# Kernel optimization log

Hardware: AMD Instinct MI355X
Metric: run time of the kernel (lower is better)

## Reference

```python
import jax, jax.numpy as jnp
import numpy as np

B, N, M, K = 4, 8192, 2048, 8
F1, F2 = 256, 256


def _knn_idx(p1t, p2t, k):
    # p1t [B,N,3], p2t [B,M,3] -> idx [B,N,k] of k nearest points in p2t for each p1t point
    d = (jnp.sum(p1t ** 2, -1)[:, :, None]
         + jnp.sum(p2t ** 2, -1)[:, None, :]
         - 2.0 * jnp.einsum('bnc,bmc->bnm', p1t, p2t))
    _, idx = jax.lax.top_k(-d, k)
    return idx


def _gather(feat, idx):
    # feat [B,C,M], idx [B,N,K] -> [B,C,N,K]  (grouping_operation)
    return jax.vmap(lambda f, i: f[:, i])(feat, idx)


def setup_inputs() -> dict:
    key = jax.random.key(0)
    ks = jax.random.split(key, 16)
    rn = lambda k, s: jax.random.normal(k, s, dtype=jnp.float32)
    ru = lambda k, s: jax.random.uniform(k, s, dtype=jnp.float32)
    return {
        'pos1': rn(ks[0], (B, 3, N)),
        'pos2': rn(ks[1], (B, 3, M)),
        'feature1': rn(ks[2], (B, F1, N)),
        'feature2': rn(ks[3], (B, F2, M)),
        'w1_0': rn(ks[4], (128, F2 + 3)) * 0.05, 's1_0': ru(ks[5], (128,)), 'b1_0': rn(ks[6], (128,)) * 0.05,
        'w1_1': rn(ks[7], (128, 128)) * 0.05, 's1_1': ru(ks[8], (128,)), 'b1_1': rn(ks[9], (128,)) * 0.05,
        'w1_2': rn(ks[10], (256, 128)) * 0.05, 's1_2': ru(ks[11], (256,)), 'b1_2': rn(ks[12], (256,)) * 0.05,
        'w2_0': rn(ks[13], (256, 256 + F1)) * 0.05, 's2_0': ru(ks[14], (256,)), 'b2_0': rn(ks[15], (256,)) * 0.05,
    }


def reference(pos1, pos2, feature1, feature2,
              w1_0, s1_0, b1_0, w1_1, s1_1, b1_1, w1_2, s1_2, b1_2,
              w2_0, s2_0, b2_0):
    # KNN grouping (knn=True branch): neighbors of each pos1 point among pos2 points
    idx = _knn_idx(pos1.transpose(0, 2, 1), pos2.transpose(0, 2, 1), K)  # [B,N,K]
    pos2_grouped = _gather(pos2, idx)                 # [B,3,N,K]
    pos_diff = pos2_grouped - pos1[:, :, :, None]     # [B,3,N,K]
    feat2_grouped = _gather(feature2, idx)            # [B,F2,N,K]
    feat = jnp.concatenate([feat2_grouped, pos_diff], axis=1)  # [B,F2+3,N,K]
    # mlp1: 1x1 Conv2d (no bias) + BN(eval, folded scale/bias) + ReLU
    for w, s, b in ((w1_0, s1_0, b1_0), (w1_1, s1_1, b1_1), (w1_2, s1_2, b1_2)):
        feat = jax.nn.relu(jnp.einsum('oc,bcnk->bonk', w, feat)
                           * s[None, :, None, None] + b[None, :, None, None])
    feat = jnp.max(feat, axis=-1)                     # [B,256,N]
    feat = jnp.concatenate([feat, feature1], axis=1)  # [B,256+F1,N]
    # mlp2: 1x1 Conv1d (no bias) + BN + ReLU
    for w, s, b in ((w2_0, s2_0, b2_0),):
        feat = jax.nn.relu(jnp.einsum('oc,bcn->bon', w, feat)
                           * s[None, :, None] + b[None, :, None])
    return feat
```

## Files before the change

### kernel.cpp

```cpp
#include <hip/hip_runtime.h>
#include <hip/hip_bf16.h>

#define B_ 4
#define N_ 8192
#define M_ 2048
#define K_ 8

typedef __bf16 bf16x8 __attribute__((ext_vector_type(8)));
typedef __bf16 bf16x4 __attribute__((ext_vector_type(4)));
typedef float  floatx4 __attribute__((ext_vector_type(4)));
typedef unsigned long long u64k;

__global__ __launch_bounds__(256) void prep_weights(
    const float* __restrict__ w10, const float* __restrict__ w11,
    const float* __restrict__ w12, const float* __restrict__ w20,
    __bf16* __restrict__ w0p, __bf16* __restrict__ w11b,
    __bf16* __restrict__ w12b, __bf16* __restrict__ w20b)
{
  int t = blockIdx.x * 256 + threadIdx.x;
  if (t < 36864) {
    int o = t / 288, c = t - o * 288;
    w0p[t] = (c < 259) ? (__bf16)w10[o * 259 + c] : (__bf16)0.0f;
  } else if (t < 53248) {
    int i = t - 36864; w11b[i] = (__bf16)w11[i];
  } else if (t < 86016) {
    int i = t - 53248; w12b[i] = (__bf16)w12[i];
  } else if (t < 217088) {
    int i = t - 86016; w20b[i] = (__bf16)w20[i];
  }
}

__global__ __launch_bounds__(256) void transpose_cast(
    const float* __restrict__ in, __bf16* __restrict__ out, int C, int L)
{
  __shared__ float tile[32][33];
  const int b = blockIdx.z;
  const int c0 = blockIdx.y * 32, l0 = blockIdx.x * 32;
  const int tx = threadIdx.x & 31, ty = threadIdx.x >> 5;
  const float* src = in + (size_t)b * C * L;
  #pragma unroll
  for (int i = 0; i < 4; i++)
    tile[ty + 8 * i][tx] = src[(size_t)(c0 + ty + 8 * i) * L + l0 + tx];
  __syncthreads();
  __bf16* dst = out + (size_t)b * L * C;
  #pragma unroll
  for (int i = 0; i < 4; i++)
    dst[(size_t)(l0 + ty + 8 * i) * C + c0 + tx] = (__bf16)tile[tx][ty + 8 * i];
}

__device__ __forceinline__ void ce(u64k& a, u64k& b) {
  u64k lo = a < b ? a : b;
  u64k hi = a < b ? b : a;
  a = lo; b = hi;
}

__global__ __launch_bounds__(256, 4) void knn_kernel(
    const float* __restrict__ pos1, const float* __restrict__ pos2,
    u64k* __restrict__ part)
{
  __shared__ floatx4 P[1024];
  __shared__ u64k md[64][33];
  const int b = blockIdx.y;
  const int half = blockIdx.z;
  const int n0 = blockIdx.x * 64;
  const int tid = threadIdx.x;
  const int cbase = half * 1024;

  const float* p2 = pos2 + b * 3 * M_;
  for (int i = tid; i < 1024; i += 256) {
    const int c = cbase + i;
    float x = p2[c], y = p2[M_ + c], z = p2[2 * M_ + c];
    floatx4 q;
    q[0] = x; q[1] = y; q[2] = z;
    q[3] = __fadd_rn(__fadd_rn(__fmul_rn(x, x), __fmul_rn(y, y)), __fmul_rn(z, z));
    P[i] = q;
  }
  __syncthreads();

  const int p = tid >> 2, t = tid & 3;
  const int n = n0 + p;
  const float* p1 = pos1 + b * 3 * N_;
  const float x1 = p1[n], y1 = p1[N_ + n], z1 = p1[2 * N_ + n];
  const float r1 = __fadd_rn(__fadd_rn(__fmul_rn(x1, x1), __fmul_rn(y1, y1)),
                             __fmul_rn(z1, z1));

  u64k bd[8];
  #pragma unroll
  for (int r = 0; r < 8; r++) bd[r] = ~0ULL;

  for (int bb = 0; bb < 32; ++bb) {
    floatx4 q[8];
    #pragma unroll
    for (int i = 0; i < 8; i++) q[i] = P[4 * (8 * bb + i) + t];

    u64k s[8];
    #pragma unroll
    for (int i = 0; i < 8; i++) {
      float dot = __fadd_rn(__fadd_rn(__fmul_rn(x1, q[i][0]), __fmul_rn(y1, q[i][1])),
                            __fmul_rn(z1, q[i][2]));
      float d = __fsub_rn(__fadd_rn(r1, q[i][3]), __fmul_rn(2.0f, dot));
      unsigned du = __float_as_uint(d);
      unsigned k32 = du ^ ((unsigned)((int)du >> 31) | 0x80000000u);
      s[i] = ((u64k)k32 << 11) | (unsigned)(cbase + 4 * (8 * bb + i) + t);
    }

    ce(s[0], s[1]); ce(s[2], s[3]); ce(s[4], s[5]); ce(s[6], s[7]);
    ce(s[0], s[2]); ce(s[1], s[3]); ce(s[4], s[6]); ce(s[5], s[7]);
    ce(s[1], s[2]); ce(s[5], s[6]);
    ce(s[0], s[4]); ce(s[1], s[5]); ce(s[2], s[6]); ce(s[3], s[7]);
    ce(s[2], s[4]); ce(s[3], s[5]);
    ce(s[1], s[2]); ce(s[3], s[4]); ce(s[5], s[6]);

    if (s[0] < bd[7]) {
      #pragma unroll
      for (int k = 0; k < 8; k++) { u64k x = s[7 - k]; bd[k] = bd[k] < x ? bd[k] : x; }
      ce(bd[0], bd[4]); ce(bd[1], bd[5]); ce(bd[2], bd[6]); ce(bd[3], bd[7]);
      ce(bd[0], bd[2]); ce(bd[1], bd[3]); ce(bd[4], bd[6]); ce(bd[5], bd[7]);
      ce(bd[0], bd[1]); ce(bd[2], bd[3]); ce(bd[4], bd[5]); ce(bd[6], bd[7]);
    }
  }

  #pragma unroll
  for (int r = 0; r < 8; r++) md[p][t * 8 + r] = bd[r];
  __syncthreads();

  if (tid < 64) {
    int h0 = 0, h1 = 0, h2 = 0, h3 = 0;
    u64k* o = part + ((size_t)((b * 2 + half) * N_ + n0 + tid)) * 8;
    #pragma unroll
    for (int r = 0; r < 8; r++) {
      u64k k0 = md[tid][h0], k1 = md[tid][8 + h1];
      u64k k2 = md[tid][16 + h2], k3 = md[tid][24 + h3];
      u64k m01 = k0 < k1 ? k0 : k1;
      u64k m23 = k2 < k3 ? k2 : k3;
      u64k m = m01 < m23 ? m01 : m23;
      h0 += (k0 == m); h1 += (k1 == m); h2 += (k2 == m); h3 += (k3 == m);
      o[r] = m;
    }
  }
}

__global__ __launch_bounds__(256) void knn_merge(
    const u64k* __restrict__ part, int* __restrict__ idx_out)
{
  const int pt = blockIdx.x * 256 + threadIdx.x;
  const int b = pt >> 13, n = pt & (N_ - 1);
  const u64k* a0 = part + ((size_t)((b * 2 + 0) * N_ + n)) * 8;
  const u64k* a1 = part + ((size_t)((b * 2 + 1) * N_ + n)) * 8;
  u64k av[8], cv[8];
  #pragma unroll
  for (int r = 0; r < 8; r++) { av[r] = a0[r]; cv[r] = a1[r]; }
  #pragma unroll
  for (int k = 0; k < 8; k++) { u64k x = cv[7 - k]; av[k] = av[k] < x ? av[k] : x; }
  ce(av[0], av[4]); ce(av[1], av[5]); ce(av[2], av[6]); ce(av[3], av[7]);
  ce(av[0], av[2]); ce(av[1], av[3]); ce(av[4], av[6]); ce(av[5], av[7]);
  ce(av[0], av[1]); ce(av[2], av[3]); ce(av[4], av[5]); ce(av[6], av[7]);
  int* o = idx_out + (size_t)pt * 8;
  #pragma unroll
  for (int r = 0; r < 8; r++) o[r] = (int)(av[r] & 2047u);
}

template <int KSTEPS>
__device__ __forceinline__ void mfma_kloop_swz(
    const __bf16* X, const __bf16* W, int wstride, int c0, int lane,
    floatx4 (&acc)[4][2])
{
  const int lrow = lane & 15, quad = lane >> 4;
  const floatx4 fz = {0.f, 0.f, 0.f, 0.f};
  #pragma unroll
  for (int pt = 0; pt < 4; pt++) { acc[pt][0] = fz; acc[pt][1] = fz; }

  bf16x8 wf0 = *(const bf16x8*)(W + (size_t)(c0 + lrow) * wstride + quad * 8);
  bf16x8 wf1 = *(const bf16x8*)(W + (size_t)(c0 + 16 + lrow) * wstride + quad * 8);
  bf16x8 xf[4];
  #pragma unroll
  for (int pt = 0; pt < 4; pt++) {
    const int row = pt * 16 + lrow;
    xf[pt] = *(const bf16x8*)((const char*)X + row * 256
                              + ((quad * 16) ^ ((row & 7) << 4)));
  }

  #pragma unroll
  for (int ks = 0; ks < KSTEPS; ks++) {
    bf16x8 wn0, wn1, xn[4];
    if (ks + 1 < KSTEPS) {
      const int kn = (ks + 1) * 32 + quad * 8;
      wn0 = *(const bf16x8*)(W + (size_t)(c0 + lrow) * wstride + kn);
      wn1 = *(const bf16x8*)(W + (size_t)(c0 + 16 + lrow) * wstride + kn);
      #pragma unroll
      for (int pt = 0; pt < 4; pt++) {
        const int row = pt * 16 + lrow;
        xn[pt] = *(const bf16x8*)((const char*)X + row * 256
                                  + (((ks + 1) * 64 + quad * 16) ^ ((row & 7) << 4)));
      }
    }
    #pragma unroll
    for (int pt = 0; pt < 4; pt++) {
      acc[pt][0] = __builtin_amdgcn_mfma_f32_16x16x32_bf16(wf0, xf[pt], acc[pt][0], 0, 0, 0);
      acc[pt][1] = __builtin_amdgcn_mfma_f32_16x16x32_bf16(wf1, xf[pt], acc[pt][1], 0, 0, 0);
    }
    if (ks + 1 < KSTEPS) {
      wf0 = wn0; wf1 = wn1;
      #pragma unroll
      for (int pt = 0; pt < 4; pt++) xf[pt] = xn[pt];
    }
  }
}

__global__ __launch_bounds__(256, 4) void mlp1_kernel(
    const float* __restrict__ pos1, const float* __restrict__ pos2,
    const int* __restrict__ idx, const __bf16* __restrict__ f2t,
    const __bf16* __restrict__ w0p, const float* __restrict__ s10, const float* __restrict__ b10,
    const __bf16* __restrict__ w11b, const float* __restrict__ s11, const float* __restrict__ b11,
    const __bf16* __restrict__ w12b, const float* __restrict__ s12, const float* __restrict__ b12,
    __bf16* __restrict__ maxed)
{
  __shared__ __align__(16) __bf16 Xs[64 * 256];
  __bf16* const Y1 = Xs;
  __bf16* const Y0 = Xs + 32 * 256;
  __bf16* const Mst = Xs + 32 * 256;

  const int b = blockIdx.y;
  const int n0 = blockIdx.x * 8;
  const int tid = threadIdx.x;
  const int wave = tid >> 6, lane = tid & 63;
  const int lrow = lane & 15, quad = lane >> 4;
  const int c0 = 32 * wave;
  const int idxbase = (b * N_ + n0) * K_;

  {
    const int r0 = wave * 16;
    const int hf = lane >> 5;
    const int ch = lane & 31;
    int mr[8];
    #pragma unroll
    for (int i = 0; i < 8; i++)
      mr[i] = idx[idxbase + r0 + 2 * i + hf];
    #pragma unroll
    for (int i = 0; i < 8; i++) {
      const int r = r0 + 2 * i + hf;
      const char* src = (const char*)f2t
          + (((size_t)(b * M_ + mr[i])) << 9)
          + ((ch << 4) ^ ((r & 7) << 4));
      __builtin_amdgcn_global_load_lds(
          (const __attribute__((address_space(1))) unsigned int*)src,
          (__attribute__((address_space(3))) unsigned int*)(Xs + (r0 + 2 * i) * 256),
          16, 0, 0);
    }
  }

  bf16x8 xlast[4];
  #pragma unroll
  for (int pt = 0; pt < 4; pt++) { bf16x8 v = {}; xlast[pt] = v; }
  if (quad == 0) {
    #pragma unroll
    for (int pt = 0; pt < 4; pt++) {
      const int r = pt * 16 + lrow;
      const int m = idx[idxbase + r];
      const int n = n0 + (r >> 3);
      bf16x8 v = {};
      v[0] = (__bf16)(pos2[b * 3 * M_ + m]          - pos1[b * 3 * N_ + n]);
      v[1] = (__bf16)(pos2[b * 3 * M_ + M_ + m]     - pos1[b * 3 * N_ + N_ + n]);
      v[2] = (__bf16)(pos2[b * 3 * M_ + 2 * M_ + m] - pos1[b * 3 * N_ + 2 * N_ + n]);
      xlast[pt] = v;
    }
  }

  bf16x8 wf0 = *(const bf16x8*)(w0p + (size_t)(c0 + lrow) * 288 + quad * 8);
  bf16x8 wf1 = *(const bf16x8*)(w0p + (size_t)(c0 + 16 + lrow) * 288 + quad * 8);

  __syncthreads();

  floatx4 acc[4][2];
  {
    const floatx4 fz = {0.f, 0.f, 0.f, 0.f};
    #pragma unroll
    for (int pt = 0; pt < 4; pt++) { acc[pt][0] = fz; acc[pt][1] = fz; }

    const int swz = (lrow & 7) << 4;
    bf16x8 xf[4];
    #pragma unroll
    for (int pt = 0; pt < 4; pt++)
      xf[pt] = *(const bf16x8*)((const char*)Xs + (pt * 16 + lrow) * 512
                                + ((quad * 16) ^ swz));

    #pragma unroll
    for (int ks = 0; ks < 9; ks++) {
      bf16x8 wn0, wn1, xn[4];
      if (ks < 8) {
        const int kn = (ks + 1) * 32 + quad * 8;
        wn0 = *(const bf16x8*)(w0p + (size_t)(c0 + lrow) * 288 + kn);
        wn1 = *(const bf16x8*)(w0p + (size_t)(c0 + 16 + lrow) * 288 + kn);
        if (ks < 7) {
          const int kb = ((ks + 1) * 64 + quad * 16) ^ swz;
          #pragma unroll
          for (int pt = 0; pt < 4; pt++)
            xn[pt] = *(const bf16x8*)((const char*)Xs + (pt * 16 + lrow) * 512 + kb);
        } else {
          #pragma unroll
          for (int pt = 0; pt < 4; pt++) xn[pt] = xlast[pt];
        }
      }
      #pragma unroll
      for (int pt = 0; pt < 4; pt++) {
        acc[pt][0] = __builtin_amdgcn_mfma_f32_16x16x32_bf16(wf0, xf[pt], acc[pt][0], 0, 0, 0);
        acc[pt][1] = __builtin_amdgcn_mfma_f32_16x16x32_bf16(wf1, xf[pt], acc[pt][1], 0, 0, 0);
      }
      if (ks < 8) {
        wf0 = wn0; wf1 = wn1;
        #pragma unroll
        for (int pt = 0; pt < 4; pt++) xf[pt] = xn[pt];
      }
    }
  }

  __syncthreads();

  #pragma unroll
  for (int pt = 0; pt < 4; pt++) {
    #pragma unroll
    for (int wt = 0; wt < 2; wt++) {
      const int colg = c0 + wt * 16 + quad * 4;
      floatx4 s4 = *(const floatx4*)(s10 + colg);
      floatx4 b4 = *(const floatx4*)(b10 + colg);
      bf16x4 pk;
      #pragma unroll
      for (int r = 0; r < 4; r++) {
        float v = acc[pt][wt][r] * s4[r] + b4[r];
        pk[r] = (__bf16)(v > 0.f ? v : 0.f);
      }
      const int row = pt * 16 + lrow;
      const int cb = colg * 2;
      *(bf16x4*)((char*)Y0 + row * 256
                 + ((cb & ~15) ^ ((row & 7) << 4)) + (cb & 15)) = pk;
    }
  }
  __syncthreads();

  {
    floatx4 a1c[4][2];
    mfma_kloop_swz<4>(Y0, w11b, 128, c0, lane, a1c);
    #pragma unroll
    for (int pt = 0; pt < 4; pt++) {
      #pragma unroll
      for (int wt = 0; wt < 2; wt++) {
        const int colg = c0 + wt * 16 + quad * 4;
        floatx4 s4 = *(const floatx4*)(s11 + colg);
        floatx4 b4 = *(const floatx4*)(b11 + colg);
        bf16x4 pk;
        #pragma unroll
        for (int r = 0; r < 4; r++) {
          float v = a1c[pt][wt][r] * s4[r] + b4[r];
          pk[r] = (__bf16)(v > 0.f ? v : 0.f);
        }
        const int row = pt * 16 + lrow;
        const int cb = colg * 2;
        *(bf16x4*)((char*)Y1 + row * 256
                   + ((cb & ~15) ^ ((row & 7) << 4)) + (cb & 15)) = pk;
      }
    }
  }
  __syncthreads();

  #pragma unroll
  for (int p = 0; p < 2; p++) {
    floatx4 a2c[4][2];
    mfma_kloop_swz<4>(Y1, w12b, 128, 128 * p + c0, lane, a2c);
    #pragma unroll
    for (int pt = 0; pt < 4; pt++) {
      #pragma unroll
      for (int wt = 0; wt < 2; wt++) {
        const int colg = 128 * p + c0 + wt * 16 + quad * 4;
        floatx4 s4 = *(const floatx4*)(s12 + colg);
        floatx4 b4 = *(const floatx4*)(b12 + colg);
        floatx4 v;
        #pragma unroll
        for (int r = 0; r < 4; r++) {
          float t = a2c[pt][wt][r] * s4[r] + b4[r];
          v[r] = t > 0.f ? t : 0.f;
        }
        #pragma unroll
        for (int st = 1; st <= 4; st <<= 1) {
          #pragma unroll
          for (int r = 0; r < 4; r++)
            v[r] = fmaxf(v[r], __shfl_xor(v[r], st, 64));
        }
        if ((lrow & 7) == 0) {
          const int point = pt * 2 + (lrow >> 3);
          bf16x4 pk;
          #pragma unroll
          for (int r = 0; r < 4; r++) pk[r] = (__bf16)v[r];
          *(bf16x4*)(Mst + point * 264 + colg) = pk;
        }
      }
    }
  }
  __syncthreads();

  {
    const int point = tid >> 5, ch = tid & 31;
    bf16x8 v = *(const bf16x8*)(Mst + point * 264 + ch * 8);
    *(bf16x8*)(maxed + ((size_t)(b * N_ + n0 + point)) * 256 + ch * 8) = v;
  }
}

__global__ __launch_bounds__(256, 6) void mlp2_kernel(
    const __bf16* __restrict__ maxed, const __bf16* __restrict__ f1t,
    const __bf16* __restrict__ w20b, const float* __restrict__ s20,
    const float* __restrict__ b20, float* __restrict__ out)
{
  const int rows0 = blockIdx.x * 32;
  const int b = rows0 >> 13;
  const int nbase = rows0 & (N_ - 1);
  const int tid = threadIdx.x;
  const int wave = tid >> 6, lane = tid & 63;
  const int lrow = lane & 15, quad = lane >> 4;
  const int c0 = 128 * blockIdx.y + 32 * wave;
  const floatx4 fz = {0.f, 0.f, 0.f, 0.f};

  floatx4 acc[2][2];
  acc[0][0] = fz; acc[0][1] = fz; acc[1][0] = fz; acc[1][1] = fz;

  auto aptr = [&](int ks, int mt) -> const __bf16* {
    const int k = ks * 32 + quad * 8;
    return (ks < 8) ? (maxed + (size_t)(rows0 + mt * 16 + lrow) * 256 + k)
                    : (f1t + (size_t)(rows0 + mt * 16 + lrow) * 256 + (k - 256));
  };

  bf16x8 w0 = *(const bf16x8*)(w20b + (size_t)(c0 + lrow) * 512 + quad * 8);
  bf16x8 w1 = *(const bf16x8*)(w20b + (size_t)(c0 + 16 + lrow) * 512 + quad * 8);
  bf16x8 a0 = *(const bf16x8*)aptr(0, 0);
  bf16x8 a1 = *(const bf16x8*)aptr(0, 1);

  #pragma unroll
  for (int ks = 0; ks < 16; ks++) {
    bf16x8 wn0, wn1, an0, an1;
    if (ks < 15) {
      const int kn = (ks + 1) * 32 + quad * 8;
      wn0 = *(const bf16x8*)(w20b + (size_t)(c0 + lrow) * 512 + kn);
      wn1 = *(const bf16x8*)(w20b + (size_t)(c0 + 16 + lrow) * 512 + kn);
      an0 = *(const bf16x8*)aptr(ks + 1, 0);
      an1 = *(const bf16x8*)aptr(ks + 1, 1);
    }
    acc[0][0] = __builtin_amdgcn_mfma_f32_16x16x32_bf16(a0, w0, acc[0][0], 0, 0, 0);
    acc[0][1] = __builtin_amdgcn_mfma_f32_16x16x32_bf16(a0, w1, acc[0][1], 0, 0, 0);
    acc[1][0] = __builtin_amdgcn_mfma_f32_16x16x32_bf16(a1, w0, acc[1][0], 0, 0, 0);
    acc[1][1] = __builtin_amdgcn_mfma_f32_16x16x32_bf16(a1, w1, acc[1][1], 0, 0, 0);
    if (ks < 15) { w0 = wn0; w1 = wn1; a0 = an0; a1 = an1; }
  }

  #pragma unroll
  for (int ct = 0; ct < 2; ct++) {
    const int col = c0 + ct * 16 + lrow;
    const float s = s20[col];
    const float bb = b20[col];
    #pragma unroll
    for (int mt = 0; mt < 2; mt++) {
      floatx4 pk;
      #pragma unroll
      for (int r = 0; r < 4; r++) {
        float v = acc[mt][ct][r] * s + bb;
        pk[r] = v > 0.f ? v : 0.f;
      }
      const int n = nbase + mt * 16 + quad * 4;
      *(floatx4*)(out + ((size_t)(b * 256 + col)) * N_ + n) = pk;
    }
  }
}

extern "C" void kernel_launch(void* const* d_in, const int* in_sizes, int n_in,
                              void* d_out, int out_size, void* d_ws, size_t ws_size,
                              hipStream_t stream)
{
  const float* pos1     = (const float*)d_in[0];
  const float* pos2     = (const float*)d_in[1];
  const float* feature1 = (const float*)d_in[2];
  const float* feature2 = (const float*)d_in[3];
  const float* w1_0 = (const float*)d_in[4];
  const float* s1_0 = (const float*)d_in[5];
  const float* b1_0 = (const float*)d_in[6];
  const float* w1_1 = (const float*)d_in[7];
  const float* s1_1 = (const float*)d_in[8];
  const float* b1_1 = (const float*)d_in[9];
  const float* w1_2 = (const float*)d_in[10];
  const float* s1_2 = (const float*)d_in[11];
  const float* b1_2 = (const float*)d_in[12];
  const float* w2_0 = (const float*)d_in[13];
  const float* s2_0 = (const float*)d_in[14];
  const float* b2_0 = (const float*)d_in[15];

  char* ws = (char*)d_ws;
  int*    idx   = (int*)(ws);
  __bf16* f2t   = (__bf16*)(ws + 1048576);
  __bf16* f1t   = (__bf16*)(ws + 5242880);
  __bf16* maxed = (__bf16*)(ws + 22020096);
  __bf16* w0p   = (__bf16*)(ws + 38797312);
  __bf16* w11b  = (__bf16*)(ws + 38871040);
  __bf16* w12b  = (__bf16*)(ws + 38903808);
  __bf16* w20b  = (__bf16*)(ws + 38969344);
  u64k*   part  = (u64k*)(ws + 22020096);

  prep_weights<<<dim3(848), 256, 0, stream>>>(w1_0, w1_1, w1_2, w2_0,
                                              w0p, w11b, w12b, w20b);
  transpose_cast<<<dim3(M_ / 32, 8, B_), 256, 0, stream>>>(feature2, f2t, 256, M_);
  transpose_cast<<<dim3(N_ / 32, 8, B_), 256, 0, stream>>>(feature1, f1t, 256, N_);
  knn_kernel<<<dim3(N_ / 64, B_, 2), 256, 0, stream>>>(pos1, pos2, part);
  knn_merge<<<dim3(N_ * B_ / 256), 256, 0, stream>>>(part, idx);
  mlp1_kernel<<<dim3(N_ / 8, B_), 256, 0, stream>>>(
      pos1, pos2, idx, f2t, w0p, s1_0, b1_0, w11b, s1_1, b1_1, w12b, s1_2, b1_2, maxed);
  mlp2_kernel<<<dim3(1024, 2), 256, 0, stream>>>(maxed, f1t, w20b, s2_0, b2_0,
                                                 (float*)d_out);
}
```

Before: 345.2 us.

## Fuse kernels: merge preprocessing, fold knn merge into mlp1, read feature1 directly

Combines the weight conversion and feature2 transpose into one preprocessing launch. Moves the two-half top-k merge into mlp1 so each block merges its own 8 points into shared memory before gathering. mlp2 now reads feature1 as fp32 straight from its original channel-major layout, so the transpose pass and the f1t buffer are gone. The goal is fewer launches and less intermediate traffic. The cost is strided, uncoalesced 8-element fp32 loads in mlp2, an extra barrier and serial merge work in mlp1, and lower occupancy hints.

Result: no change. 344.9 us (-0.1%).

```diff
diff --git a/kernel.cpp b/kernel.cpp
--- a/kernel.cpp
+++ b/kernel.cpp
@@ -11,41 +11,43 @@
 typedef float  floatx4 __attribute__((ext_vector_type(4)));
 typedef unsigned long long u64k;
 
-__global__ __launch_bounds__(256) void prep_weights(
+__global__ __launch_bounds__(256) void preproc(
     const float* __restrict__ w10, const float* __restrict__ w11,
     const float* __restrict__ w12, const float* __restrict__ w20,
+    const float* __restrict__ feature2,
     __bf16* __restrict__ w0p, __bf16* __restrict__ w11b,
-    __bf16* __restrict__ w12b, __bf16* __restrict__ w20b)
-{
-  int t = blockIdx.x * 256 + threadIdx.x;
-  if (t < 36864) {
-    int o = t / 288, c = t - o * 288;
-    w0p[t] = (c < 259) ? (__bf16)w10[o * 259 + c] : (__bf16)0.0f;
-  } else if (t < 53248) {
-    int i = t - 36864; w11b[i] = (__bf16)w11[i];
-  } else if (t < 86016) {
-    int i = t - 53248; w12b[i] = (__bf16)w12[i];
-  } else if (t < 217088) {
-    int i = t - 86016; w20b[i] = (__bf16)w20[i];
-  }
-}
-
-__global__ __launch_bounds__(256) void transpose_cast(
-    const float* __restrict__ in, __bf16* __restrict__ out, int C, int L)
+    __bf16* __restrict__ w12b, __bf16* __restrict__ w20b,
+    __bf16* __restrict__ f2t)
 {
   __shared__ float tile[32][33];
-  const int b = blockIdx.z;
-  const int c0 = blockIdx.y * 32, l0 = blockIdx.x * 32;
-  const int tx = threadIdx.x & 31, ty = threadIdx.x >> 5;
-  const float* src = in + (size_t)b * C * L;
-  #pragma unroll
-  for (int i = 0; i < 4; i++)
-    tile[ty + 8 * i][tx] = src[(size_t)(c0 + ty + 8 * i) * L + l0 + tx];
-  __syncthreads();
-  __bf16* dst = out + (size_t)b * L * C;
-  #pragma unroll
-  for (int i = 0; i < 4; i++)
-    dst[(size_t)(l0 + ty + 8 * i) * C + c0 + tx] = (__bf16)tile[tx][ty + 8 * i];
+  const int bid = blockIdx.x;
+  if (bid < 2048) {
+    const int C = 256, L = M_;
+    const int b = bid >> 9;
+    const int c0 = ((bid >> 6) & 7) * 32, l0 = (bid & 63) * 32;
+    const int tx = threadIdx.x & 31, ty = threadIdx.x >> 5;
+    const float* src = feature2 + (size_t)b * C * L;
+    #pragma unroll
+    for (int i = 0; i < 4; i++)
+      tile[ty + 8 * i][tx] = src[(size_t)(c0 + ty + 8 * i) * L + l0 + tx];
+    __syncthreads();
+    __bf16* dst = f2t + (size_t)b * L * C;
+    #pragma unroll
+    for (int i = 0; i < 4; i++)
+      dst[(size_t)(l0 + ty + 8 * i) * C + c0 + tx] = (__bf16)tile[tx][ty + 8 * i];
+  } else {
+    int t = (bid - 2048) * 256 + threadIdx.x;
+    if (t < 36864) {
+      int o = t / 288, c = t - o * 288;
+      w0p[t] = (c < 259) ? (__bf16)w10[o * 259 + c] : (__bf16)0.0f;
+    } else if (t < 53248) {
+      int i = t - 36864; w11b[i] = (__bf16)w11[i];
+    } else if (t < 86016) {
+      int i = t - 53248; w12b[i] = (__bf16)w12[i];
+    } else if (t < 217088) {
+      int i = t - 86016; w20b[i] = (__bf16)w20[i];
+    }
+  }
 }
 
 __device__ __forceinline__ void ce(u64k& a, u64k& b) {
@@ -140,26 +142,6 @@
   }
 }
 
-__global__ __launch_bounds__(256) void knn_merge(
-    const u64k* __restrict__ part, int* __restrict__ idx_out)
-{
-  const int pt = blockIdx.x * 256 + threadIdx.x;
-  const int b = pt >> 13, n = pt & (N_ - 1);
-  const u64k* a0 = part + ((size_t)((b * 2 + 0) * N_ + n)) * 8;
-  const u64k* a1 = part + ((size_t)((b * 2 + 1) * N_ + n)) * 8;
-  u64k av[8], cv[8];
-  #pragma unroll
-  for (int r = 0; r < 8; r++) { av[r] = a0[r]; cv[r] = a1[r]; }
-  #pragma unroll
-  for (int k = 0; k < 8; k++) { u64k x = cv[7 - k]; av[k] = av[k] < x ? av[k] : x; }
-  ce(av[0], av[4]); ce(av[1], av[5]); ce(av[2], av[6]); ce(av[3], av[7]);
-  ce(av[0], av[2]); ce(av[1], av[3]); ce(av[4], av[6]); ce(av[5], av[7]);
-  ce(av[0], av[1]); ce(av[2], av[3]); ce(av[4], av[5]); ce(av[6], av[7]);
-  int* o = idx_out + (size_t)pt * 8;
-  #pragma unroll
-  for (int r = 0; r < 8; r++) o[r] = (int)(av[r] & 2047u);
-}
-
 template <int KSTEPS>
 __device__ __forceinline__ void mfma_kloop_swz(
     const __bf16* X, const __bf16* W, int wstride, int c0, int lane,
@@ -207,15 +189,16 @@
   }
 }
 
-__global__ __launch_bounds__(256, 4) void mlp1_kernel(
+__global__ __launch_bounds__(256, 3) void mlp1_kernel(
     const float* __restrict__ pos1, const float* __restrict__ pos2,
-    const int* __restrict__ idx, const __bf16* __restrict__ f2t,
+    const u64k* __restrict__ part, const __bf16* __restrict__ f2t,
     const __bf16* __restrict__ w0p, const float* __restrict__ s10, const float* __restrict__ b10,
     const __bf16* __restrict__ w11b, const float* __restrict__ s11, const float* __restrict__ b11,
     const __bf16* __restrict__ w12b, const float* __restrict__ s12, const float* __restrict__ b12,
     __bf16* __restrict__ maxed)
 {
   __shared__ __align__(16) __bf16 Xs[64 * 256];
+  __shared__ int mrow[64];
   __bf16* const Y1 = Xs;
   __bf16* const Y0 = Xs + 32 * 256;
   __bf16* const Mst = Xs + 32 * 256;
@@ -226,21 +209,33 @@
   const int wave = tid >> 6, lane = tid & 63;
   const int lrow = lane & 15, quad = lane >> 4;
   const int c0 = 32 * wave;
-  const int idxbase = (b * N_ + n0) * K_;
+
+  if (tid < 8) {
+    const u64k* a0 = part + ((size_t)((b * 2 + 0) * N_ + n0 + tid)) * 8;
+    const u64k* a1 = part + ((size_t)((b * 2 + 1) * N_ + n0 + tid)) * 8;
+    u64k av[8], cv[8];
+    #pragma unroll
+    for (int r = 0; r < 8; r++) { av[r] = a0[r]; cv[r] = a1[r]; }
+    #pragma unroll
+    for (int k = 0; k < 8; k++) { u64k x = cv[7 - k]; av[k] = av[k] < x ? av[k] : x; }
+    ce(av[0], av[4]); ce(av[1], av[5]); ce(av[2], av[6]); ce(av[3], av[7]);
+    ce(av[0], av[2]); ce(av[1], av[3]); ce(av[4], av[6]); ce(av[5], av[7]);
+    ce(av[0], av[1]); ce(av[2], av[3]); ce(av[4], av[5]); ce(av[6], av[7]);
+    #pragma unroll
+    for (int r = 0; r < 8; r++) mrow[tid * 8 + r] = (int)(av[r] & 2047u);
+  }
+  __syncthreads();
 
   {
     const int r0 = wave * 16;
     const int hf = lane >> 5;
     const int ch = lane & 31;
-    int mr[8];
-    #pragma unroll
-    for (int i = 0; i < 8; i++)
-      mr[i] = idx[idxbase + r0 + 2 * i + hf];
     #pragma unroll
     for (int i = 0; i < 8; i++) {
       const int r = r0 + 2 * i + hf;
+      const int m = mrow[r];
       const char* src = (const char*)f2t
-          + (((size_t)(b * M_ + mr[i])) << 9)
+          + (((size_t)(b * M_ + m)) << 9)
           + ((ch << 4) ^ ((r & 7) << 4));
       __builtin_amdgcn_global_load_lds(
           (const __attribute__((address_space(1))) unsigned int*)src,
@@ -256,7 +251,7 @@
     #pragma unroll
     for (int pt = 0; pt < 4; pt++) {
       const int r = pt * 16 + lrow;
-      const int m = idx[idxbase + r];
+      const int m = mrow[r];
       const int n = n0 + (r >> 3);
       bf16x8 v = {};
       v[0] = (__bf16)(pos2[b * 3 * M_ + m]          - pos1[b * 3 * N_ + n]);
@@ -404,8 +399,8 @@
   }
 }
 
-__global__ __launch_bounds__(256, 6) void mlp2_kernel(
-    const __bf16* __restrict__ maxed, const __bf16* __restrict__ f1t,
+__global__ __launch_bounds__(256, 4) void mlp2_kernel(
+    const __bf16* __restrict__ maxed, const float* __restrict__ feature1,
     const __bf16* __restrict__ w20b, const float* __restrict__ s20,
     const float* __restrict__ b20, float* __restrict__ out)
 {
@@ -421,16 +416,25 @@
   floatx4 acc[2][2];
   acc[0][0] = fz; acc[0][1] = fz; acc[1][0] = fz; acc[1][1] = fz;
 
-  auto aptr = [&](int ks, int mt) -> const __bf16* {
+  auto afrag = [&](int ks, int mt) -> bf16x8 {
     const int k = ks * 32 + quad * 8;
-    return (ks < 8) ? (maxed + (size_t)(rows0 + mt * 16 + lrow) * 256 + k)
-                    : (f1t + (size_t)(rows0 + mt * 16 + lrow) * 256 + (k - 256));
+    if (ks < 8) {
+      return *(const bf16x8*)(maxed + (size_t)(rows0 + mt * 16 + lrow) * 256 + k);
+    } else {
+      const int c = k - 256;
+      const float* p = feature1 + ((size_t)(b * 256 + c)) * N_
+                       + (nbase + mt * 16 + lrow);
+      bf16x8 v;
+      #pragma unroll
+      for (int j = 0; j < 8; j++) v[j] = (__bf16)p[(size_t)j * N_];
+      return v;
+    }
   };
 
   bf16x8 w0 = *(const bf16x8*)(w20b + (size_t)(c0 + lrow) * 512 + quad * 8);
   bf16x8 w1 = *(const bf16x8*)(w20b + (size_t)(c0 + 16 + lrow) * 512 + quad * 8);
-  bf16x8 a0 = *(const bf16x8*)aptr(0, 0);
-  bf16x8 a1 = *(const bf16x8*)aptr(0, 1);
+  bf16x8 a0 = afrag(0, 0);
+  bf16x8 a1 = afrag(0, 1);
 
   #pragma unroll
   for (int ks = 0; ks < 16; ks++) {
@@ -439,8 +443,8 @@
       const int kn = (ks + 1) * 32 + quad * 8;
       wn0 = *(const bf16x8*)(w20b + (size_t)(c0 + lrow) * 512 + kn);
       wn1 = *(const bf16x8*)(w20b + (size_t)(c0 + 16 + lrow) * 512 + kn);
-      an0 = *(const bf16x8*)aptr(ks + 1, 0);
-      an1 = *(const bf16x8*)aptr(ks + 1, 1);
+      an0 = afrag(ks + 1, 0);
+      an1 = afrag(ks + 1, 1);
     }
     acc[0][0] = __builtin_amdgcn_mfma_f32_16x16x32_bf16(a0, w0, acc[0][0], 0, 0, 0);
     acc[0][1] = __builtin_amdgcn_mfma_f32_16x16x32_bf16(a0, w1, acc[0][1], 0, 0, 0);
@@ -490,24 +494,19 @@
   const float* b2_0 = (const float*)d_in[15];
 
   char* ws = (char*)d_ws;
-  int*    idx   = (int*)(ws);
   __bf16* f2t   = (__bf16*)(ws + 1048576);
-  __bf16* f1t   = (__bf16*)(ws + 5242880);
+  u64k*   part  = (u64k*)(ws + 5242880);
   __bf16* maxed = (__bf16*)(ws + 22020096);
   __bf16* w0p   = (__bf16*)(ws + 38797312);
   __bf16* w11b  = (__bf16*)(ws + 38871040);
   __bf16* w12b  = (__bf16*)(ws + 38903808);
   __bf16* w20b  = (__bf16*)(ws + 38969344);
-  u64k*   part  = (u64k*)(ws + 22020096);
-
-  prep_weights<<<dim3(848), 256, 0, stream>>>(w1_0, w1_1, w1_2, w2_0,
-                                              w0p, w11b, w12b, w20b);
-  transpose_cast<<<dim3(M_ / 32, 8, B_), 256, 0, stream>>>(feature2, f2t, 256, M_);
-  transpose_cast<<<dim3(N_ / 32, 8, B_), 256, 0, stream>>>(feature1, f1t, 256, N_);
+
+  preproc<<<dim3(2896), 256, 0, stream>>>(w1_0, w1_1, w1_2, w2_0, feature2,
+                                          w0p, w11b, w12b, w20b, f2t);
   knn_kernel<<<dim3(N_ / 64, B_, 2), 256, 0, stream>>>(pos1, pos2, part);
-  knn_merge<<<dim3(N_ * B_ / 256), 256, 0, stream>>>(part, idx);
   mlp1_kernel<<<dim3(N_ / 8, B_), 256, 0, stream>>>(
-      pos1, pos2, idx, f2t, w0p, s1_0, b1_0, w11b, s1_1, b1_1, w12b, s1_2, b1_2, maxed);
-  mlp2_kernel<<<dim3(1024, 2), 256, 0, stream>>>(maxed, f1t, w20b, s2_0, b2_0,
+      pos1, pos2, part, f2t, w0p, s1_0, b1_0, w11b, s1_1, b1_1, w12b, s1_2, b1_2, maxed);
+  mlp2_kernel<<<dim3(1024, 2), 256, 0, stream>>>(maxed, feature1, w20b, s2_0, b2_0,
                                                  (float*)d_out);
 }
```

## Merge preprocessing kernels with KNN and stage mlp2 activations in LDS

Applied to the files above, without the earlier changes.

Folds the weight-cast, two feature transposes and the KNN top-k into one heterogeneous launch, dispatched by block index, so the independent work overlaps and several launches disappear. Adds an XOR swizzle to the KNN merge scratch to reduce LDS bank conflicts. Restructures mlp2 so each block computes all 256 output channels for 32 rows, loading the A tile into swizzled LDS once via global_load_lds rather than having two blocks each read it from global. This raises per-thread accumulators and lowers the occupancy bound from 6 to 3, and the bigger combined kernel may see uneven tail scheduling.

Result: faster. 306.0 us (-11.3%).

```diff
diff --git a/kernel.cpp b/kernel.cpp
--- a/kernel.cpp
+++ b/kernel.cpp
@@ -11,42 +11,8 @@
 typedef float  floatx4 __attribute__((ext_vector_type(4)));
 typedef unsigned long long u64k;
 
-__global__ __launch_bounds__(256) void prep_weights(
-    const float* __restrict__ w10, const float* __restrict__ w11,
-    const float* __restrict__ w12, const float* __restrict__ w20,
-    __bf16* __restrict__ w0p, __bf16* __restrict__ w11b,
-    __bf16* __restrict__ w12b, __bf16* __restrict__ w20b)
-{
-  int t = blockIdx.x * 256 + threadIdx.x;
-  if (t < 36864) {
-    int o = t / 288, c = t - o * 288;
-    w0p[t] = (c < 259) ? (__bf16)w10[o * 259 + c] : (__bf16)0.0f;
-  } else if (t < 53248) {
-    int i = t - 36864; w11b[i] = (__bf16)w11[i];
-  } else if (t < 86016) {
-    int i = t - 53248; w12b[i] = (__bf16)w12[i];
-  } else if (t < 217088) {
-    int i = t - 86016; w20b[i] = (__bf16)w20[i];
-  }
-}
-
-__global__ __launch_bounds__(256) void transpose_cast(
-    const float* __restrict__ in, __bf16* __restrict__ out, int C, int L)
-{
-  __shared__ float tile[32][33];
-  const int b = blockIdx.z;
-  const int c0 = blockIdx.y * 32, l0 = blockIdx.x * 32;
-  const int tx = threadIdx.x & 31, ty = threadIdx.x >> 5;
-  const float* src = in + (size_t)b * C * L;
-  #pragma unroll
-  for (int i = 0; i < 4; i++)
-    tile[ty + 8 * i][tx] = src[(size_t)(c0 + ty + 8 * i) * L + l0 + tx];
-  __syncthreads();
-  __bf16* dst = out + (size_t)b * L * C;
-  #pragma unroll
-  for (int i = 0; i < 4; i++)
-    dst[(size_t)(l0 + ty + 8 * i) * C + c0 + tx] = (__bf16)tile[tx][ty + 8 * i];
-}
+#define AS1G __attribute__((address_space(1)))
+#define AS3L __attribute__((address_space(3)))
 
 __device__ __forceinline__ void ce(u64k& a, u64k& b) {
   u64k lo = a < b ? a : b;
@@ -54,88 +20,149 @@
   a = lo; b = hi;
 }
 
-__global__ __launch_bounds__(256, 4) void knn_kernel(
+__global__ __launch_bounds__(256) void pre_knn(
+    const float* __restrict__ w10, const float* __restrict__ w11,
+    const float* __restrict__ w12, const float* __restrict__ w20,
+    const float* __restrict__ feature1, const float* __restrict__ feature2,
     const float* __restrict__ pos1, const float* __restrict__ pos2,
+    __bf16* __restrict__ w0p, __bf16* __restrict__ w11b,
+    __bf16* __restrict__ w12b, __bf16* __restrict__ w20b,
+    __bf16* __restrict__ f2t, __bf16* __restrict__ f1t,
     u64k* __restrict__ part)
 {
-  __shared__ floatx4 P[1024];
-  __shared__ u64k md[64][33];
-  const int b = blockIdx.y;
-  const int half = blockIdx.z;
-  const int n0 = blockIdx.x * 64;
+  __shared__ __align__(16) char smem[32768];
+  const int bid = blockIdx.x;
   const int tid = threadIdx.x;
-  const int cbase = half * 1024;
-
-  const float* p2 = pos2 + b * 3 * M_;
-  for (int i = tid; i < 1024; i += 256) {
-    const int c = cbase + i;
-    float x = p2[c], y = p2[M_ + c], z = p2[2 * M_ + c];
-    floatx4 q;
-    q[0] = x; q[1] = y; q[2] = z;
-    q[3] = __fadd_rn(__fadd_rn(__fmul_rn(x, x), __fmul_rn(y, y)), __fmul_rn(z, z));
-    P[i] = q;
-  }
-  __syncthreads();
-
-  const int p = tid >> 2, t = tid & 3;
-  const int n = n0 + p;
-  const float* p1 = pos1 + b * 3 * N_;
-  const float x1 = p1[n], y1 = p1[N_ + n], z1 = p1[2 * N_ + n];
-  const float r1 = __fadd_rn(__fadd_rn(__fmul_rn(x1, x1), __fmul_rn(y1, y1)),
-                             __fmul_rn(z1, z1));
-
-  u64k bd[8];
-  #pragma unroll
-  for (int r = 0; r < 8; r++) bd[r] = ~0ULL;
-
-  for (int bb = 0; bb < 32; ++bb) {
-    floatx4 q[8];
-    #pragma unroll
-    for (int i = 0; i < 8; i++) q[i] = P[4 * (8 * bb + i) + t];
-
-    u64k s[8];
-    #pragma unroll
-    for (int i = 0; i < 8; i++) {
-      float dot = __fadd_rn(__fadd_rn(__fmul_rn(x1, q[i][0]), __fmul_rn(y1, q[i][1])),
-                            __fmul_rn(z1, q[i][2]));
-      float d = __fsub_rn(__fadd_rn(r1, q[i][3]), __fmul_rn(2.0f, dot));
-      unsigned du = __float_as_uint(d);
-      unsigned k32 = du ^ ((unsigned)((int)du >> 31) | 0x80000000u);
-      s[i] = ((u64k)k32 << 11) | (unsigned)(cbase + 4 * (8 * bb + i) + t);
-    }
-
-    ce(s[0], s[1]); ce(s[2], s[3]); ce(s[4], s[5]); ce(s[6], s[7]);
-    ce(s[0], s[2]); ce(s[1], s[3]); ce(s[4], s[6]); ce(s[5], s[7]);
-    ce(s[1], s[2]); ce(s[5], s[6]);
-    ce(s[0], s[4]); ce(s[1], s[5]); ce(s[2], s[6]); ce(s[3], s[7]);
-    ce(s[2], s[4]); ce(s[3], s[5]);
-    ce(s[1], s[2]); ce(s[3], s[4]); ce(s[5], s[6]);
-
-    if (s[0] < bd[7]) {
-      #pragma unroll
-      for (int k = 0; k < 8; k++) { u64k x = s[7 - k]; bd[k] = bd[k] < x ? bd[k] : x; }
-      ce(bd[0], bd[4]); ce(bd[1], bd[5]); ce(bd[2], bd[6]); ce(bd[3], bd[7]);
-      ce(bd[0], bd[2]); ce(bd[1], bd[3]); ce(bd[4], bd[6]); ce(bd[5], bd[7]);
-      ce(bd[0], bd[1]); ce(bd[2], bd[3]); ce(bd[4], bd[5]); ce(bd[6], bd[7]);
-    }
-  }
-
-  #pragma unroll
-  for (int r = 0; r < 8; r++) md[p][t * 8 + r] = bd[r];
-  __syncthreads();
-
-  if (tid < 64) {
-    int h0 = 0, h1 = 0, h2 = 0, h3 = 0;
-    u64k* o = part + ((size_t)((b * 2 + half) * N_ + n0 + tid)) * 8;
-    #pragma unroll
-    for (int r = 0; r < 8; r++) {
-      u64k k0 = md[tid][h0], k1 = md[tid][8 + h1];
-      u64k k2 = md[tid][16 + h2], k3 = md[tid][24 + h3];
-      u64k m01 = k0 < k1 ? k0 : k1;
-      u64k m23 = k2 < k3 ? k2 : k3;
-      u64k m = m01 < m23 ? m01 : m23;
-      h0 += (k0 == m); h1 += (k1 == m); h2 += (k2 == m); h3 += (k3 == m);
-      o[r] = m;
+
+  if (bid < 1024) {
+    floatx4* P = (floatx4*)smem;
+    u64k (*md)[32] = (u64k(*)[32])(smem + 16384);
+    const int b = (bid >> 7) & 3;
+    const int half = bid >> 9;
+    const int n0 = (bid & 127) * 64;
+    const int cbase = half * 1024;
+
+    const float* p2 = pos2 + b * 3 * M_;
+    for (int i = tid; i < 1024; i += 256) {
+      const int c = cbase + i;
+      float x = p2[c], y = p2[M_ + c], z = p2[2 * M_ + c];
+      floatx4 q;
+      q[0] = x; q[1] = y; q[2] = z;
+      q[3] = __fadd_rn(__fadd_rn(__fmul_rn(x, x), __fmul_rn(y, y)), __fmul_rn(z, z));
+      P[i] = q;
+    }
+    __syncthreads();
+
+    const int p = tid >> 2, t = tid & 3;
+    const int n = n0 + p;
+    const float* p1 = pos1 + b * 3 * N_;
+    const float x1 = p1[n], y1 = p1[N_ + n], z1 = p1[2 * N_ + n];
+    const float r1 = __fadd_rn(__fadd_rn(__fmul_rn(x1, x1), __fmul_rn(y1, y1)),
+                               __fmul_rn(z1, z1));
+
+    u64k bd[8];
+    #pragma unroll
+    for (int r = 0; r < 8; r++) bd[r] = ~0ULL;
+
+    for (int bb = 0; bb < 32; ++bb) {
+      floatx4 q[8];
+      #pragma unroll
+      for (int i = 0; i < 8; i++) q[i] = P[4 * (8 * bb + i) + t];
+
+      u64k s[8];
+      #pragma unroll
+      for (int i = 0; i < 8; i++) {
+        float dot = __fadd_rn(__fadd_rn(__fmul_rn(x1, q[i][0]), __fmul_rn(y1, q[i][1])),
+                              __fmul_rn(z1, q[i][2]));
+        float d = __fsub_rn(__fadd_rn(r1, q[i][3]), __fmul_rn(2.0f, dot));
+        unsigned du = __float_as_uint(d);
+        unsigned k32 = du ^ ((unsigned)((int)du >> 31) | 0x80000000u);
+        s[i] = ((u64k)k32 << 11) | (unsigned)(cbase + 4 * (8 * bb + i) + t);
+      }
+
+      ce(s[0], s[1]); ce(s[2], s[3]); ce(s[4], s[5]); ce(s[6], s[7]);
+      ce(s[0], s[2]); ce(s[1], s[3]); ce(s[4], s[6]); ce(s[5], s[7]);
+      ce(s[1], s[2]); ce(s[5], s[6]);
+      ce(s[0], s[4]); ce(s[1], s[5]); ce(s[2], s[6]); ce(s[3], s[7]);
+      ce(s[2], s[4]); ce(s[3], s[5]);
+      ce(s[1], s[2]); ce(s[3], s[4]); ce(s[5], s[6]);
+
+      if (s[0] < bd[7]) {
+        #pragma unroll
+        for (int k = 0; k < 8; k++) { u64k x = s[7 - k]; bd[k] = bd[k] < x ? bd[k] : x; }
+        ce(bd[0], bd[4]); ce(bd[1], bd[5]); ce(bd[2], bd[6]); ce(bd[3], bd[7]);
+        ce(bd[0], bd[2]); ce(bd[1], bd[3]); ce(bd[4], bd[6]); ce(bd[5], bd[7]);
+        ce(bd[0], bd[1]); ce(bd[2], bd[3]); ce(bd[4], bd[5]); ce(bd[6], bd[7]);
+      }
+    }
+
+    {
+      const int swp = (p & 3) << 3;
+      #pragma unroll
+      for (int r = 0; r < 8; r++) md[p][(t * 8 + r) ^ swp] = bd[r];
+    }
+    __syncthreads();
+
+    if (tid < 64) {
+      const int sw = tid & 3;
+      const int b0 = (0 ^ sw) << 3, b1 = (1 ^ sw) << 3;
+      const int b2 = (2 ^ sw) << 3, b3 = (3 ^ sw) << 3;
+      int h0 = 0, h1 = 0, h2 = 0, h3 = 0;
+      u64k* o = part + ((size_t)((b * 2 + half) * N_ + n0 + tid)) * 8;
+      #pragma unroll
+      for (int r = 0; r < 8; r++) {
+        u64k k0 = md[tid][b0 + h0], k1 = md[tid][b1 + h1];
+        u64k k2 = md[tid][b2 + h2], k3 = md[tid][b3 + h3];
+        u64k m01 = k0 < k1 ? k0 : k1;
+        u64k m23 = k2 < k3 ? k2 : k3;
+        u64k m = m01 < m23 ? m01 : m23;
+        h0 += (k0 == m); h1 += (k1 == m); h2 += (k2 == m); h3 += (k3 == m);
+        o[r] = m;
+      }
+    }
+  } else if (bid < 3072) {
+    float (*tile)[33] = (float(*)[33])smem;
+    const int tb = bid - 1024;
+    const int C = 256, L = M_;
+    const int b = tb >> 9;
+    const int c0 = ((tb >> 6) & 7) * 32, l0 = (tb & 63) * 32;
+    const int tx = tid & 31, ty = tid >> 5;
+    const float* src = feature2 + (size_t)b * C * L;
+    #pragma unroll
+    for (int i = 0; i < 4; i++)
+      tile[ty + 8 * i][tx] = src[(size_t)(c0 + ty + 8 * i) * L + l0 + tx];
+    __syncthreads();
+    __bf16* dst = f2t + (size_t)b * L * C;
+    #pragma unroll
+    for (int i = 0; i < 4; i++)
+      dst[(size_t)(l0 + ty + 8 * i) * C + c0 + tx] = (__bf16)tile[tx][ty + 8 * i];
+  } else if (bid < 11264) {
+    float (*tile)[33] = (float(*)[33])smem;
+    const int tb = bid - 3072;
+    const int C = 256, L = N_;
+    const int b = tb >> 11;
+    const int c0 = ((tb >> 8) & 7) * 32, l0 = (tb & 255) * 32;
+    const int tx = tid & 31, ty = tid >> 5;
+    const float* src = feature1 + (size_t)b * C * L;
+    #pragma unroll
+    for (int i = 0; i < 4; i++)
+      tile[ty + 8 * i][tx] = src[(size_t)(c0 + ty + 8 * i) * L + l0 + tx];
+    __syncthreads();
+    __bf16* dst = f1t + (size_t)b * L * C;
+    #pragma unroll
+    for (int i = 0; i < 4; i++)
+      dst[(size_t)(l0 + ty + 8 * i) * C + c0 + tx] = (__bf16)tile[tx][ty + 8 * i];
+  } else {
+    int t = (bid - 11264) * 256 + tid;
+    if (t < 36864) {
+      int o = t / 288, c = t - o * 288;
+      w0p[t] = (c < 259) ? (__bf16)w10[o * 259 + c] : (__bf16)0.0f;
+    } else if (t < 53248) {
+      int i = t - 36864; w11b[i] = (__bf16)w11[i];
+    } else if (t < 86016) {
+      int i = t - 53248; w12b[i] = (__bf16)w12[i];
+    } else if (t < 217088) {
+      int i = t - 86016; w20b[i] = (__bf16)w20[i];
     }
   }
 }
@@ -243,8 +270,8 @@
           + (((size_t)(b * M_ + mr[i])) << 9)
           + ((ch << 4) ^ ((r & 7) << 4));
       __builtin_amdgcn_global_load_lds(
-          (const __attribute__((address_space(1))) unsigned int*)src,
-          (__attribute__((address_space(3))) unsigned int*)(Xs + (r0 + 2 * i) * 256),
+          (const AS1G unsigned int*)src,
+          (AS3L unsigned int*)(Xs + (r0 + 2 * i) * 256),
           16, 0, 0);
     }
   }
@@ -404,54 +431,87 @@
   }
 }
 
-__global__ __launch_bounds__(256, 6) void mlp2_kernel(
+__global__ __launch_bounds__(256, 3) void mlp2_kernel(
     const __bf16* __restrict__ maxed, const __bf16* __restrict__ f1t,
     const __bf16* __restrict__ w20b, const float* __restrict__ s20,
     const float* __restrict__ b20, float* __restrict__ out)
 {
+  __shared__ __align__(16) __bf16 As[2][32 * 256];
   const int rows0 = blockIdx.x * 32;
   const int b = rows0 >> 13;
   const int nbase = rows0 & (N_ - 1);
   const int tid = threadIdx.x;
   const int wave = tid >> 6, lane = tid & 63;
   const int lrow = lane & 15, quad = lane >> 4;
-  const int c0 = 128 * blockIdx.y + 32 * wave;
+  const int c0 = 64 * wave;
+
+  {
+    const int r0 = wave * 8;
+    const int hf = lane >> 5, ch = lane & 31;
+    #pragma unroll
+    for (int i = 0; i < 4; i++) {
+      const int r = r0 + 2 * i + hf;
+      const size_t srow = ((size_t)(rows0 + r)) << 9;
+      const int so = (ch << 4) ^ ((r & 7) << 4);
+      __builtin_amdgcn_global_load_lds(
+          (const AS1G unsigned int*)((const char*)maxed + srow + so),
+          (AS3L unsigned int*)(&As[0][(r0 + 2 * i) * 256]), 16, 0, 0);
+      __builtin_amdgcn_global_load_lds(
+          (const AS1G unsigned int*)((const char*)f1t + srow + so),
+          (AS3L unsigned int*)(&As[1][(r0 + 2 * i) * 256]), 16, 0, 0);
+    }
+  }
+
+  bf16x8 wf[4];
+  #pragma unroll
+  for (int wt = 0; wt < 4; wt++)
+    wf[wt] = *(const bf16x8*)(w20b + (size_t)(c0 + wt * 16 + lrow) * 512 + quad * 8);
+
+  __syncthreads();
+
+  floatx4 acc[2][4];
   const floatx4 fz = {0.f, 0.f, 0.f, 0.f};
-
-  floatx4 acc[2][2];
-  acc[0][0] = fz; acc[0][1] = fz; acc[1][0] = fz; acc[1][1] = fz;
-
-  auto aptr = [&](int ks, int mt) -> const __bf16* {
-    const int k = ks * 32 + quad * 8;
-    return (ks < 8) ? (maxed + (size_t)(rows0 + mt * 16 + lrow) * 256 + k)
-                    : (f1t + (size_t)(rows0 + mt * 16 + lrow) * 256 + (k - 256));
+  #pragma unroll
+  for (int mt = 0; mt < 2; mt++)
+    #pragma unroll
+    for (int wt = 0; wt < 4; wt++) acc[mt][wt] = fz;
+
+  auto aaddr = [&](int ks, int mt) -> const char* {
+    const int row = mt * 16 + lrow;
+    return (const char*)(&As[ks >> 3][0]) + row * 512
+           + ((((ks & 7) * 64) + quad * 16) ^ ((row & 7) << 4));
   };
 
-  bf16x8 w0 = *(const bf16x8*)(w20b + (size_t)(c0 + lrow) * 512 + quad * 8);
-  bf16x8 w1 = *(const bf16x8*)(w20b + (size_t)(c0 + 16 + lrow) * 512 + quad * 8);
-  bf16x8 a0 = *(const bf16x8*)aptr(0, 0);
-  bf16x8 a1 = *(const bf16x8*)aptr(0, 1);
+  bf16x8 af[2];
+  af[0] = *(const bf16x8*)aaddr(0, 0);
+  af[1] = *(const bf16x8*)aaddr(0, 1);
 
   #pragma unroll
   for (int ks = 0; ks < 16; ks++) {
-    bf16x8 wn0, wn1, an0, an1;
+    bf16x8 wn[4], an[2];
     if (ks < 15) {
       const int kn = (ks + 1) * 32 + quad * 8;
-      wn0 = *(const bf16x8*)(w20b + (size_t)(c0 + lrow) * 512 + kn);
-      wn1 = *(const bf16x8*)(w20b + (size_t)(c0 + 16 + lrow) * 512 + kn);
-      an0 = *(const bf16x8*)aptr(ks + 1, 0);
-      an1 = *(const bf16x8*)aptr(ks + 1, 1);
-    }
-    acc[0][0] = __builtin_amdgcn_mfma_f32_16x16x32_bf16(a0, w0, acc[0][0], 0, 0, 0);
-    acc[0][1] = __builtin_amdgcn_mfma_f32_16x16x32_bf16(a0, w1, acc[0][1], 0, 0, 0);
-    acc[1][0] = __builtin_amdgcn_mfma_f32_16x16x32_bf16(a1, w0, acc[1][0], 0, 0, 0);
-    acc[1][1] = __builtin_amdgcn_mfma_f32_16x16x32_bf16(a1, w1, acc[1][1], 0, 0, 0);
-    if (ks < 15) { w0 = wn0; w1 = wn1; a0 = an0; a1 = an1; }
-  }
-
-  #pragma unroll
-  for (int ct = 0; ct < 2; ct++) {
-    const int col = c0 + ct * 16 + lrow;
+      #pragma unroll
+      for (int wt = 0; wt < 4; wt++)
+        wn[wt] = *(const bf16x8*)(w20b + (size_t)(c0 + wt * 16 + lrow) * 512 + kn);
+      an[0] = *(const bf16x8*)aaddr(ks + 1, 0);
+      an[1] = *(const bf16x8*)aaddr(ks + 1, 1);
+    }
+    #pragma unroll
+    for (int mt = 0; mt < 2; mt++)
+      #pragma unroll
+      for (int wt = 0; wt < 4; wt++)
+        acc[mt][wt] = __builtin_amdgcn_mfma_f32_16x16x32_bf16(af[mt], wf[wt], acc[mt][wt], 0, 0, 0);
+    if (ks < 15) {
+      #pragma unroll
+      for (int wt = 0; wt < 4; wt++) wf[wt] = wn[wt];
+      af[0] = an[0]; af[1] = an[1];
+    }
+  }
+
+  #pragma unroll
+  for (int wt = 0; wt < 4; wt++) {
+    const int col = c0 + wt * 16 + lrow;
     const float s = s20[col];
     const float bb = b20[col];
     #pragma unroll
@@ -459,7 +519,7 @@
       floatx4 pk;
       #pragma unroll
       for (int r = 0; r < 4; r++) {
-        float v = acc[mt][ct][r] * s + bb;
+        float v = acc[mt][wt][r] * s + bb;
         pk[r] = v > 0.f ? v : 0.f;
       }
       const int n = nbase + mt * 16 + quad * 4;
@@ -500,14 +560,12 @@
   __bf16* w20b  = (__bf16*)(ws + 38969344);
   u64k*   part  = (u64k*)(ws + 22020096);
 
-  prep_weights<<<dim3(848), 256, 0, stream>>>(w1_0, w1_1, w1_2, w2_0,
-                                              w0p, w11b, w12b, w20b);
-  transpose_cast<<<dim3(M_ / 32, 8, B_), 256, 0, stream>>>(feature2, f2t, 256, M_);
-  transpose_cast<<<dim3(N_ / 32, 8, B_), 256, 0, stream>>>(feature1, f1t, 256, N_);
-  knn_kernel<<<dim3(N_ / 64, B_, 2), 256, 0, stream>>>(pos1, pos2, part);
+  pre_knn<<<dim3(12112), 256, 0, stream>>>(
+      w1_0, w1_1, w1_2, w2_0, feature1, feature2, pos1, pos2,
+      w0p, w11b, w12b, w20b, f2t, f1t, part);
   knn_merge<<<dim3(N_ * B_ / 256), 256, 0, stream>>>(part, idx);
   mlp1_kernel<<<dim3(N_ / 8, B_), 256, 0, stream>>>(
       pos1, pos2, idx, f2t, w0p, s1_0, b1_0, w11b, s1_1, b1_1, w12b, s1_2, b1_2, maxed);
-  mlp2_kernel<<<dim3(1024, 2), 256, 0, stream>>>(maxed, f1t, w20b, s2_0, b2_0,
-                                                 (float*)d_out);
-}
+  mlp2_kernel<<<dim3(N_ * B_ / 32), 256, 0, stream>>>(maxed, f1t, w20b, s2_0, b2_0,
+                                                      (float*)d_out);
+}
```
